# Performance work log

Hardware: AMD Instinct MI355X
Metric: run time of the kernel (lower is better)

The kernel has to match this reference:

```python
import jax, jax.numpy as jnp
import numpy as np

B, S, D = 2, 2048, 2048
H, KV, HD = 32, 8, 64          # n_heads, n_kv_heads, head_dim
NREP = H // KV                 # GQA repeat factor
ROPE_THETA = 500000.0          # llama3 base


def setup_inputs() -> dict:
    key = jax.random.key(0)
    ks = jax.random.split(key, 5)
    scale = 1.0 / np.sqrt(D)
    x = jax.random.normal(ks[0], (B, S, D), dtype=jnp.float32)
    wq = jax.random.normal(ks[1], (D, H * HD), dtype=jnp.float32) * scale
    wk = jax.random.normal(ks[2], (D, KV * HD), dtype=jnp.float32) * scale
    wv = jax.random.normal(ks[3], (D, KV * HD), dtype=jnp.float32) * scale
    wo = jax.random.normal(ks[4], (H * HD, D), dtype=jnp.float32) * scale
    # real rotary freqs, matching precompute_freqs_cis: angle[t, j] = t / theta^(2j/HD)
    inv_freq = 1.0 / (ROPE_THETA ** (np.arange(0, HD, 2, dtype=np.float32) / HD))
    t = np.arange(S, dtype=np.float32)
    ang = np.outer(t, inv_freq)  # (S, HD//2)
    freqs_cos = jnp.asarray(np.cos(ang), dtype=jnp.float32)
    freqs_sin = jnp.asarray(np.sin(ang), dtype=jnp.float32)
    return {"x": x, "wq": wq, "wk": wk, "wv": wv, "wo": wo,
            "freqs_cos": freqs_cos, "freqs_sin": freqs_sin}


def _apply_rope(t, cos, sin):
    # t: (B, S, nh, HD); pairs (even, odd) = (real, imag) of complex number
    tr = t.reshape(*t.shape[:-1], HD // 2, 2)
    re, im = tr[..., 0], tr[..., 1]
    c = cos[None, :, None, :]   # (1, S, 1, HD//2)
    s = sin[None, :, None, :]
    out_re = re * c - im * s
    out_im = re * s + im * c
    return jnp.stack([out_re, out_im], axis=-1).reshape(t.shape)


def reference(x, wq, wk, wv, wo, freqs_cos, freqs_sin):
    bsz, seq_len, _ = x.shape
    xq = (x @ wq).reshape(bsz, seq_len, H, HD)
    xk = (x @ wk).reshape(bsz, seq_len, KV, HD)
    xv = (x @ wv).reshape(bsz, seq_len, KV, HD)
    xq = _apply_rope(xq, freqs_cos, freqs_sin)
    xk = _apply_rope(xk, freqs_cos, freqs_sin)
    # GQA without materializing repeated KV: group query heads by KV head
    q = xq.transpose(0, 2, 1, 3).reshape(bsz, KV, NREP, seq_len, HD)  # bgrqh
    k = xk.transpose(0, 2, 1, 3)                                      # bgkh over seq k
    v = xv.transpose(0, 2, 1, 3)
    scores = jnp.einsum("bgrqh,bgkh->bgrqk", q, k) / jnp.sqrt(jnp.float32(HD))
    causal = jnp.tril(jnp.ones((seq_len, seq_len), dtype=bool))
    scores = jnp.where(causal[None, None, None], scores, -jnp.inf)
    probs = jax.nn.softmax(scores.astype(jnp.float32), axis=-1).astype(q.dtype)
    out = jnp.einsum("bgrqk,bgkh->bgrqh", probs, v)
    out = out.reshape(bsz, H, seq_len, HD).transpose(0, 2, 1, 3).reshape(bsz, seq_len, H * HD)
    return out @ wo
```

## Files before the change

### kernel.cpp

```cpp
#include <hip/hip_runtime.h>
#include <hip/hip_bf16.h>

typedef __attribute__((ext_vector_type(8))) short bf16x8;
typedef __attribute__((ext_vector_type(4))) float f32x4;
typedef __attribute__((ext_vector_type(16))) float f32x16;

#define S_LEN 2048
#define DMODEL 2048
#define NH 32
#define NKV 8
#define HDIM 64
#define NQKV 3072
#define BROWS 4096
#define LOG2E 1.4426950408889634f

__device__ __forceinline__ float bf2f(unsigned short u) {
    union { unsigned int i; float f; } v; v.i = ((unsigned int)u) << 16; return v.f;
}
__device__ __forceinline__ unsigned short f2bf(float f) {
    union { float f; unsigned int i; } v; v.f = f;
    unsigned int r = v.i + 0x7fffu + ((v.i >> 16) & 1u);
    return (unsigned short)(r >> 16);
}

__device__ __forceinline__ unsigned cvtpk_bf16(float lo, float hi) {
    unsigned r;
    asm("v_cvt_pk_bf16_f32 %0, %1, %2" : "=v"(r) : "v"(lo), "v"(hi));
    return r;
}
__device__ __forceinline__ void pl32swap(unsigned &a, unsigned &b) {
    asm("v_permlane32_swap_b32 %0, %1" : "+v"(a), "+v"(b));
}
__device__ __forceinline__ float exp2_fast(float x) {
    float r;
    asm("v_exp_f32 %0, %1" : "=v"(r) : "v"(x));
    return r;
}

__device__ __forceinline__ void gload_lds16(const void* g, void* l) {
    __builtin_amdgcn_global_load_lds(
        (const __attribute__((address_space(1))) unsigned int*)(unsigned long long)g,
        (__attribute__((address_space(3))) unsigned int*)(unsigned int)(unsigned long long)l,
        16, 0, 0);
}

#define VMW(n) asm volatile("s_waitcnt vmcnt(" #n ")" ::: "memory")
#define LGW()  asm volatile("s_waitcnt lgkmcnt(0)" ::: "memory")
#define CFENCE() asm volatile("" ::: "memory")

__global__ __launch_bounds__(256) void prep_kernel(
    const float* __restrict__ x,
    const float* __restrict__ wq, const float* __restrict__ wk,
    const float* __restrict__ wv, const float* __restrict__ wo,
    unsigned short* __restrict__ xb,
    unsigned short* __restrict__ wqkvT,
    unsigned short* __restrict__ woT) {
    int bid = blockIdx.x;
    if (bid < 8192) {
        int idx = bid * 256 + threadIdx.x;
        float4 v = ((const float4*)x)[idx];
        ushort4 o;
        o.x = f2bf(v.x); o.y = f2bf(v.y); o.z = f2bf(v.z); o.w = f2bf(v.w);
        ((ushort4*)xb)[idx] = o;
        return;
    }
    bid -= 8192;
    const float* src;
    unsigned short* dst;
    int N, nx;
    if (bid < 4096)      { src = wq; dst = wqkvT;                                N = 2048; nx = 64; }
    else if (bid < 5120) { bid -= 4096; src = wk; dst = wqkvT + (size_t)2048 * DMODEL; N = 512; nx = 16; }
    else if (bid < 6144) { bid -= 5120; src = wv; dst = wqkvT + (size_t)2560 * DMODEL; N = 512; nx = 16; }
    else                 { bid -= 6144; src = wo; dst = woT;                     N = 2048; nx = 64; }
    const int K = DMODEL;
    const int n0 = (bid % nx) * 32, k0 = (bid / nx) * 32;
    __shared__ float t[32][33];
    const int tx = threadIdx.x & 31, ty = threadIdx.x >> 5;
#pragma unroll
    for (int i = 0; i < 32; i += 8)
        t[ty + i][tx] = src[(size_t)(k0 + ty + i) * N + n0 + tx];
    __syncthreads();
#pragma unroll
    for (int i = 0; i < 32; i += 8)
        dst[(size_t)(n0 + ty + i) * K + k0 + tx] = f2bf(t[tx][ty + i]);
}

__global__ void vtrans_kernel(const unsigned short* __restrict__ qkv,
                              unsigned short* __restrict__ vt) {
    __shared__ unsigned short t[32][33];
    int s0 = blockIdx.x * 32;
    int hd0 = (blockIdx.y & 1) * 32;
    int bg = blockIdx.y >> 1;
    int b = bg >> 3, g = bg & 7;
    int tx = threadIdx.x & 31, ty = threadIdx.x >> 5;
#pragma unroll
    for (int i = 0; i < 32; i += 8)
        t[ty + i][tx] = qkv[(size_t)(b * S_LEN + s0 + ty + i) * NQKV + 2560 + g * 64 + hd0 + tx];
    __syncthreads();
#pragma unroll
    for (int i = 0; i < 32; i += 8)
        vt[(size_t)(bg * 64 + hd0 + ty + i) * S_LEN + s0 + tx] = t[tx][ty + i];
}

template <int NJF, int OUTF32, int ROPE>
__global__ __launch_bounds__(512, 2) void gemm_wide_kernel(
    const unsigned short* __restrict__ A,
    const unsigned short* __restrict__ BT,
    void* __restrict__ Cv,
    const float* __restrict__ fc, const float* __restrict__ fs,
    int M, int N, int K, int nbx) {
    extern __shared__ __align__(16) unsigned short lds[];
    const int ABUF = 8192;
    const int BSTRIDE = NJF * 4096;
    const int BBASE = 2 * ABUF;

    const int nwg = gridDim.x;
    const int cpx = nwg >> 3;
    const int swz = ((int)blockIdx.x & 7) * cpx + ((int)blockIdx.x >> 3);
    const int m0 = (swz / nbx) * 128, n0 = (swz % nbx) * (NJF * 64);

    const int tid = threadIdx.x;
    const int lane = tid & 63, wid = tid >> 6;
    const int wr = wid >> 2, wc = wid & 3;
    const int l16 = lane & 15, lg = lane >> 4;

    const int sr0 = tid >> 3, sk0 = tid & 7;
    const int kc = (sk0 ^ (sr0 & 7)) * 8;
    const size_t K64 = (size_t)64 * K;
    const unsigned short* gA = A + (size_t)(m0 + sr0) * K + kc;
    const unsigned short* gB = BT + (size_t)(n0 + sr0) * K + kc;
    unsigned short* ldsA = lds + tid * 8;
    unsigned short* ldsB = lds + BBASE + tid * 8;

    f32x4 acc[4][NJF];
#pragma unroll
    for (int i = 0; i < 4; ++i)
#pragma unroll
        for (int j = 0; j < NJF; ++j)
#pragma unroll
            for (int e = 0; e < 4; ++e) acc[i][j][e] = 0.f;

    const int NT = K >> 6;
    {
        gload_lds16(gA, ldsA);
        gload_lds16(gA + K64, ldsA + 4096);
#pragma unroll
        for (int j = 0; j < NJF; ++j)
            gload_lds16(gB + (size_t)j * K64, ldsB + j * 4096);
    }

    for (int t = 0; t < NT; ++t) {
        const int cur = t & 1, nxt = cur ^ 1;
        if (t + 1 < NT) {
            gload_lds16(gA + 64, ldsA + nxt * ABUF);
            gload_lds16(gA + 64 + K64, ldsA + nxt * ABUF + 4096);
#pragma unroll
            for (int j = 0; j < NJF; ++j)
                gload_lds16(gB + 64 + (size_t)j * K64, ldsB + nxt * BSTRIDE + j * 4096);
            if constexpr (NJF == 6) { VMW(8); } else { VMW(6); }
        } else {
            VMW(0);
        }
        __builtin_amdgcn_s_barrier();
        CFENCE();

#pragma unroll
        for (int ks = 0; ks < 2; ++ks) {
            bf16x8 af[4], bfv[NJF];
#pragma unroll
            for (int mi = 0; mi < 4; ++mi) {
                const int rA = wr * 64 + mi * 16 + l16;
                af[mi] = *(const bf16x8*)(lds + cur * ABUF + rA * 64 + ((ks * 4 + lg) ^ (rA & 7)) * 8);
            }
#pragma unroll
            for (int nj = 0; nj < NJF; ++nj) {
                const int rB = nj * 64 + wc * 16 + l16;
                bfv[nj] = *(const bf16x8*)(lds + BBASE + cur * BSTRIDE + rB * 64 + ((ks * 4 + lg) ^ (rB & 7)) * 8);
            }
#pragma unroll
            for (int mi = 0; mi < 4; ++mi)
#pragma unroll
                for (int nj = 0; nj < NJF; ++nj)
                    acc[mi][nj] = __builtin_amdgcn_mfma_f32_16x16x32_bf16(
                        af[mi], bfv[nj], acc[mi][nj], 0, 0, 0);
        }
        CFENCE();
        LGW();
        __builtin_amdgcn_s_barrier();
        CFENCE();
        gA += 64;
        gB += 64;
    }

    const float QS = 0.125f * LOG2E;
    const int fidx = (wc * 16 + l16) >> 1;
    const bool evenl = !(l16 & 1);
#pragma unroll
    for (int mi = 0; mi < 4; ++mi) {
        const int row = m0 + wr * 64 + mi * 16 + lg * 4;
#pragma unroll
        for (int e = 0; e < 4; ++e) {
            if (OUTF32) {
                float* Cf = (float*)Cv;
#pragma unroll
                for (int nj = 0; nj < NJF; ++nj)
                    Cf[(size_t)(row + e) * N + n0 + nj * 64 + wc * 16 + l16] = acc[mi][nj][e];
            } else if (!ROPE) {
                unsigned short* Cb = (unsigned short*)Cv;
#pragma unroll
                for (int nj = 0; nj < NJF; ++nj)
                    Cb[(size_t)(row + e) * N + n0 + nj * 64 + wc * 16 + l16] = f2bf(acc[mi][nj][e]);
            } else {
                unsigned short* Cb = (unsigned short*)Cv;
                const int seq = (row + e) & (S_LEN - 1);
                const float c = fc[seq * 32 + fidx], s = fs[seq * 32 + fidx];
#pragma unroll
                for (int nj = 0; nj < NJF; ++nj) {
                    const int cbase = n0 + nj * 64 + wc * 16;
                    float v = acc[mi][nj][e];
                    float o;
                    if (cbase >= 2560) {
                        o = v;
                    } else {
                        float p = __shfl_xor(v, 1);
                        o = fmaf(v, c, evenl ? -(p * s) : (p * s));
                        if (cbase < 2048) o *= QS;
                    }
                    Cb[(size_t)(row + e) * N + cbase + l16] = f2bf(o);
                }
            }
        }
    }
}

template <int OUTF32>
__global__ __launch_bounds__(256) void gemm_bt_kernel(
    const unsigned short* __restrict__ A,
    const unsigned short* __restrict__ BT,
    void* __restrict__ Cv,
    int M, int N, int K) {
    __shared__ __align__(16) unsigned short Als[128 * 32];
    __shared__ __align__(16) unsigned short Bls[128 * 32];

    const int tid = threadIdx.x;
    const int lane = tid & 63;
    const int wid = tid >> 6;
    const int wr = wid >> 1, wc = wid & 1;
    const int l16 = lane & 15, lg = lane >> 4;
    const int m0 = blockIdx.y * 128, n0 = blockIdx.x * 128;

    f32x4 acc[4][4];
#pragma unroll
    for (int i = 0; i < 4; ++i)
#pragma unroll
        for (int j = 0; j < 4; ++j)
#pragma unroll
            for (int e = 0; e < 4; ++e) acc[i][j][e] = 0.f;

    const int f0 = tid, f1 = 256 + tid;
    const int ar0 = f0 >> 2, ac0 = (f0 & 3) * 8;
    const int ar1 = f1 >> 2, ac1 = (f1 & 3) * 8;
    const size_t Abase = (size_t)m0 * K;
    const size_t Bbase = (size_t)n0 * K;

    for (int k0 = 0; k0 < K; k0 += 32) {
        __syncthreads();
        gload_lds16(A + Abase + (size_t)ar0 * K + k0 + ac0, Als + f0 * 8);
        gload_lds16(A + Abase + (size_t)ar1 * K + k0 + ac1, Als + f1 * 8);
        gload_lds16(BT + Bbase + (size_t)ar0 * K + k0 + ac0, Bls + f0 * 8);
        gload_lds16(BT + Bbase + (size_t)ar1 * K + k0 + ac1, Bls + f1 * 8);
        __syncthreads();
        bf16x8 af[4], bfv[4];
#pragma unroll
        for (int i = 0; i < 4; ++i)
            af[i] = *(const bf16x8*)(Als + (wr * 64 + i * 16 + l16) * 32 + lg * 8);
#pragma unroll
        for (int j = 0; j < 4; ++j)
            bfv[j] = *(const bf16x8*)(Bls + (wc * 64 + j * 16 + l16) * 32 + lg * 8);
#pragma unroll
        for (int i = 0; i < 4; ++i)
#pragma unroll
            for (int j = 0; j < 4; ++j)
                acc[i][j] = __builtin_amdgcn_mfma_f32_16x16x32_bf16(af[i], bfv[j], acc[i][j], 0, 0, 0);
    }

    const int row_base = m0 + wr * 64 + lg * 4;
    const int col_base = n0 + wc * 64 + l16;
    if (OUTF32) {
        float* Cf = (float*)Cv;
#pragma unroll
        for (int i = 0; i < 4; ++i)
#pragma unroll
            for (int r = 0; r < 4; ++r)
#pragma unroll
                for (int j = 0; j < 4; ++j)
                    Cf[(size_t)(row_base + i * 16 + r) * N + col_base + j * 16] = acc[i][j][r];
    } else {
        unsigned short* Cb = (unsigned short*)Cv;
#pragma unroll
        for (int i = 0; i < 4; ++i)
#pragma unroll
            for (int r = 0; r < 4; ++r)
#pragma unroll
                for (int j = 0; j < 4; ++j)
                    Cb[(size_t)(row_base + i * 16 + r) * N + col_base + j * 16] = f2bf(acc[i][j][r]);
    }
}

__global__ void rope_kernel(unsigned short* __restrict__ qkv,
                            const float* __restrict__ fc, const float* __restrict__ fs) {
    const int PAIRS = 1280;
    int idx = blockIdx.x * blockDim.x + threadIdx.x;
    int row = idx / PAIRS;
    int w = idx - row * PAIRS;
    int s = row & (S_LEN - 1);
    int col = (w < 1024) ? (w * 2) : (2048 + (w - 1024) * 2);
    int f = (col & 63) >> 1;
    float c = fc[s * 32 + f], sn = fs[s * 32 + f];
    unsigned int* p = (unsigned int*)(qkv + (size_t)row * NQKV + col);
    unsigned int v = *p;
    float re = bf2f((unsigned short)(v & 0xffffu));
    float im = bf2f((unsigned short)(v >> 16));
    float oro = re * c - im * sn;
    float oim = re * sn + im * c;
    if (w < 1024) { oro *= 0.125f * LOG2E; oim *= 0.125f * LOG2E; }
    *p = (unsigned int)f2bf(oro) | ((unsigned int)f2bf(oim) << 16);
}

__global__ __launch_bounds__(512) void attn_kernel(
    const unsigned short* __restrict__ qkv,
    const unsigned short* __restrict__ vt,
    unsigned short* __restrict__ aout) {
    __shared__ __align__(16) unsigned short Kls[2][64 * 64];
    __shared__ __align__(16) unsigned short Vls[2][64 * 64];
    __shared__ float Fbuf[8][32];

    const int tid = threadIdx.x, lane = tid & 63, wid = tid >> 6;
    const int l31 = lane & 31, hi = lane >> 5;
    const int g = blockIdx.x, b = blockIdx.y;
    const int h = g * 4 + (wid & 3);
    const int cw = wid >> 2;

    const int srow = tid >> 3, schk = tid & 7;
    const int sc = schk ^ (srow & 7);
    const unsigned short* kgs = qkv + (size_t)(b * S_LEN + srow) * NQKV + 2048 + g * 64 + sc * 8;
    const unsigned short* vgs = vt + (size_t)((b * 8 + g) * 64 + srow) * S_LEN + sc * 8;
    const int dd = tid * 8;

    const int xr = l31 & 7;

    const int z = 31 - (int)blockIdx.z;
    const int chunk = 2 * z + cw;
    const int q0 = chunk * 32;
    const int ntiles = z + 1;
    const int qg_row = q0 + l31;

    bf16x8 qf[4];
    {
        const unsigned short* qp =
            qkv + (size_t)(b * S_LEN + q0 + l31) * NQKV + h * HDIM + hi * 8;
#pragma unroll
        for (int s = 0; s < 4; ++s) qf[s] = *(const bf16x8*)(qp + s * 16);
    }

    float l_r = 0.f;
    f32x16 oacc0, oacc1;
#pragma unroll
    for (int r = 0; r < 16; ++r) { oacc0[r] = 0.f; oacc1[r] = 0.f; }

    gload_lds16(kgs, Kls[0] + dd);
    gload_lds16(vgs, Vls[0] + dd);
    __syncthreads();

    for (int t = 0; t < ntiles; ++t) {
        const int kv0 = t * 64;
        if (t + 1 < ntiles) {
            const int nkv = kv0 + 64;
            gload_lds16(kgs + (size_t)nkv * NQKV, Kls[(t + 1) & 1] + dd);
            gload_lds16(vgs + nkv, Vls[(t + 1) & 1] + dd);
        }
        const unsigned short* Kb = Kls[t & 1];
        const unsigned short* Vb = Vls[t & 1];

        f32x16 s0, s1;
#pragma unroll
        for (int r = 0; r < 16; ++r) { s0[r] = 0.f; s1[r] = 0.f; }
        __builtin_amdgcn_s_setprio(1);
#pragma unroll
        for (int s = 0; s < 4; ++s) {
            const int coff = ((s * 2 + hi) ^ xr) * 8;
            bf16x8 kf0 = *(const bf16x8*)(Kb + l31 * 64 + coff);
            bf16x8 kf1 = *(const bf16x8*)(Kb + (32 + l31) * 64 + coff);
            s0 = __builtin_amdgcn_mfma_f32_32x32x16_bf16(kf0, qf[s], s0, 0, 0, 0);
            s1 = __builtin_amdgcn_mfma_f32_32x32x16_bf16(kf1, qf[s], s1, 0, 0, 0);
        }
        __builtin_amdgcn_s_setprio(0);
        if (t == ntiles - 1) {
#pragma unroll
            for (int r = 0; r < 16; ++r) {
                int kvr = kv0 + (r & 3) + 8 * (r >> 2) + 4 * hi;
                if (kvr > qg_row) s0[r] = -3.0e38f;
                if (kvr + 32 > qg_row) s1[r] = -3.0e38f;
            }
        }
        float r0 = 0.f, r1 = 0.f, r2 = 0.f, r3 = 0.f;
#pragma unroll
        for (int r = 0; r < 16; r += 4) {
            s0[r + 0] = exp2_fast(s0[r + 0]); r0 += s0[r + 0];
            s0[r + 1] = exp2_fast(s0[r + 1]); r1 += s0[r + 1];
            s0[r + 2] = exp2_fast(s0[r + 2]); r2 += s0[r + 2];
            s0[r + 3] = exp2_fast(s0[r + 3]); r3 += s0[r + 3];
        }
#pragma unroll
        for (int r = 0; r < 16; r += 4) {
            s1[r + 0] = exp2_fast(s1[r + 0]); r0 += s1[r + 0];
            s1[r + 1] = exp2_fast(s1[r + 1]); r1 += s1[r + 1];
            s1[r + 2] = exp2_fast(s1[r + 2]); r2 += s1[r + 2];
            s1[r + 3] = exp2_fast(s1[r + 3]); r3 += s1[r + 3];
        }
        l_r += (r0 + r1) + (r2 + r3);

        unsigned pw[4][4];
#define BUILD_PA(c, S, base)                                    \
        {                                                       \
            unsigned x0 = cvtpk_bf16(S[base + 0], S[base + 1]); \
            unsigned y0 = cvtpk_bf16(S[base + 4], S[base + 5]); \
            pl32swap(x0, y0);                                   \
            unsigned x1 = cvtpk_bf16(S[base + 2], S[base + 3]); \
            unsigned y1 = cvtpk_bf16(S[base + 6], S[base + 7]); \
            pl32swap(x1, y1);                                   \
            pw[c][0] = x0; pw[c][1] = x1; pw[c][2] = y0; pw[c][3] = y1; \
        }
        BUILD_PA(0, s0, 0)
        BUILD_PA(1, s0, 8)
        BUILD_PA(2, s1, 0)
        BUILD_PA(3, s1, 8)
#undef BUILD_PA

        __builtin_amdgcn_s_setprio(1);
#pragma unroll
        for (int c = 0; c < 4; ++c) {
            union { unsigned u[4]; bf16x8 v; } pa;
            pa.u[0] = pw[c][0]; pa.u[1] = pw[c][1]; pa.u[2] = pw[c][2]; pa.u[3] = pw[c][3];
            const int coff = ((c * 2 + hi) ^ xr) * 8;
            bf16x8 vf0 = *(const bf16x8*)(Vb + l31 * 64 + coff);
            bf16x8 vf1 = *(const bf16x8*)(Vb + (32 + l31) * 64 + coff);
            oacc0 = __builtin_amdgcn_mfma_f32_32x32x16_bf16(pa.v, vf0, oacc0, 0, 0, 0);
            oacc1 = __builtin_amdgcn_mfma_f32_32x32x16_bf16(pa.v, vf1, oacc1, 0, 0, 0);
        }
        __builtin_amdgcn_s_setprio(0);
        __syncthreads();
    }

    l_r += __shfl_xor(l_r, 32);
    if (lane < 32) Fbuf[wid][l31] = 1.0f / l_r;
    asm volatile("s_waitcnt lgkmcnt(0)" ::: "memory");
#pragma unroll
    for (int rg = 0; rg < 4; ++rg) {
#pragma unroll
        for (int rr = 0; rr < 4; ++rr) {
            int row = 8 * rg + 4 * hi + rr;
            float inv = Fbuf[wid][row];
            int r = rg * 4 + rr;
            size_t orow = (size_t)(b * S_LEN + q0 + row) * DMODEL + h * HDIM;
            aout[orow + l31] = f2bf(oacc0[r] * inv);
            aout[orow + 32 + l31] = f2bf(oacc1[r] * inv);
        }
    }
}

extern "C" void kernel_launch(void* const* d_in, const int* in_sizes, int n_in,
                              void* d_out, int out_size, void* d_ws, size_t ws_size,
                              hipStream_t stream) {
    const float* x = (const float*)d_in[0];
    const float* wq = (const float*)d_in[1];
    const float* wk = (const float*)d_in[2];
    const float* wv = (const float*)d_in[3];
    const float* wo = (const float*)d_in[4];
    const float* fc = (const float*)d_in[5];
    const float* fs = (const float*)d_in[6];
    float* out = (float*)d_out;

    unsigned short* xb = (unsigned short*)d_ws;
    unsigned short* wqkvT = xb + (size_t)BROWS * DMODEL;
    unsigned short* woT = wqkvT + (size_t)NQKV * DMODEL;
    unsigned short* qkvb = woT + (size_t)DMODEL * DMODEL;
    unsigned short* aoutb = xb;
    unsigned short* vtb = wqkvT;

    hipError_t e1 = hipFuncSetAttribute(
        reinterpret_cast<const void*>(&gemm_wide_kernel<6, 0, 1>),
        hipFuncAttributeMaxDynamicSharedMemorySize, 131072);
    hipError_t e2 = hipFuncSetAttribute(
        reinterpret_cast<const void*>(&gemm_wide_kernel<4, 1, 0>),
        hipFuncAttributeMaxDynamicSharedMemorySize, 98304);
    const bool big = (e1 == hipSuccess && e2 == hipSuccess);

    prep_kernel<<<18432, 256, 0, stream>>>(x, wq, wk, wv, wo, xb, wqkvT, woT);
    if (big) {
        gemm_wide_kernel<6, 0, 1><<<(BROWS / 128) * (NQKV / 384), 512, 131072, stream>>>(
            xb, wqkvT, qkvb, fc, fs, BROWS, NQKV, DMODEL, NQKV / 384);
    } else {
        gemm_bt_kernel<0><<<dim3(NQKV / 128, BROWS / 128), 256, 0, stream>>>(
            xb, wqkvT, qkvb, BROWS, NQKV, DMODEL);
        rope_kernel<<<(BROWS * 1280) / 256, 256, 0, stream>>>(qkvb, fc, fs);
    }
    vtrans_kernel<<<dim3(S_LEN / 32, 32), 256, 0, stream>>>(qkvb, vtb);
    attn_kernel<<<dim3(NKV, 2, 32), 512, 0, stream>>>(qkvb, vtb, aoutb);
    if (big)
        gemm_wide_kernel<4, 1, 0><<<(BROWS / 128) * (DMODEL / 256), 512, 98304, stream>>>(
            aoutb, woT, out, nullptr, nullptr, BROWS, DMODEL, DMODEL, DMODEL / 256);
    else
        gemm_bt_kernel<1><<<dim3(DMODEL / 128, BROWS / 128), 256, 0, stream>>>(
            aoutb, woT, out, BROWS, DMODEL, DMODEL);
}
```

Before: 168.1 us.

## Halve GEMM K-tile to 32 with new LDS swizzle to cut shared memory

Reworks the wide GEMM kernel to stage K in chunks of 32 instead of 64. Each thread now loads one 16-byte chunk per 128 rows, and the LDS layout uses a swizzle adapted to 32-element rows. This halves dynamic LDS per workgroup (65536/49152 bytes), which may let more workgroups stay resident. The cost is twice as many loop iterations and barriers per K, with less MFMA work between synchronizations.

```diff
diff --git a/kernel.cpp b/kernel.cpp
--- a/kernel.cpp
+++ b/kernel.cpp
@@ -103,16 +103,17 @@
 }
 
 template <int NJF, int OUTF32, int ROPE>
-__global__ __launch_bounds__(512, 2) void gemm_wide_kernel(
+__global__ __launch_bounds__(512, 2) void gemm_w32_kernel(
     const unsigned short* __restrict__ A,
     const unsigned short* __restrict__ BT,
     void* __restrict__ Cv,
     const float* __restrict__ fc, const float* __restrict__ fs,
     int M, int N, int K, int nbx) {
     extern __shared__ __align__(16) unsigned short lds[];
-    const int ABUF = 8192;
-    const int BSTRIDE = NJF * 4096;
-    const int BBASE = 2 * ABUF;
+    constexpr int ABUF = 4096;
+    constexpr int BSTRIDE = NJF * 2048;
+    constexpr int BBASE = 2 * ABUF;
+    constexpr int NBL = NJF / 2;
 
     const int nwg = gridDim.x;
     const int cpx = nwg >> 3;
@@ -124,13 +125,18 @@
     const int wr = wid >> 2, wc = wid & 3;
     const int l16 = lane & 15, lg = lane >> 4;
 
-    const int sr0 = tid >> 3, sk0 = tid & 7;
-    const int kc = (sk0 ^ (sr0 & 7)) * 8;
-    const size_t K64 = (size_t)64 * K;
-    const unsigned short* gA = A + (size_t)(m0 + sr0) * K + kc;
-    const unsigned short* gB = BT + (size_t)(n0 + sr0) * K + kc;
-    unsigned short* ldsA = lds + tid * 8;
-    unsigned short* ldsB = lds + BBASE + tid * 8;
+    const int sr = tid >> 2, sk = tid & 3;
+    const int kc = (sk ^ ((sr >> 1) & 3)) * 8;
+    const size_t K128 = (size_t)128 * K;
+    const unsigned short* gA = A + (size_t)(m0 + sr) * K + kc;
+    const unsigned short* gB = BT + (size_t)(n0 + sr) * K + kc;
+
+#define WSTAGE(P, buf) do { \
+    gload_lds16(gA + (P), lds + (buf) * ABUF + tid * 8); \
+    _Pragma("unroll") for (int j = 0; j < NBL; ++j) \
+        gload_lds16(gB + (P) + (size_t)j * K128, \
+                    lds + BBASE + (buf) * BSTRIDE + j * 4096 + tid * 8); \
+} while (0)
 
     f32x4 acc[4][NJF];
 #pragma unroll
@@ -140,56 +146,41 @@
 #pragma unroll
             for (int e = 0; e < 4; ++e) acc[i][j][e] = 0.f;
 
-    const int NT = K >> 6;
-    {
-        gload_lds16(gA, ldsA);
-        gload_lds16(gA + K64, ldsA + 4096);
-#pragma unroll
-        for (int j = 0; j < NJF; ++j)
-            gload_lds16(gB + (size_t)j * K64, ldsB + j * 4096);
-    }
+    const int NT = K >> 5;
+    WSTAGE(0, 0);
 
     for (int t = 0; t < NT; ++t) {
         const int cur = t & 1, nxt = cur ^ 1;
         if (t + 1 < NT) {
-            gload_lds16(gA + 64, ldsA + nxt * ABUF);
-            gload_lds16(gA + 64 + K64, ldsA + nxt * ABUF + 4096);
-#pragma unroll
-            for (int j = 0; j < NJF; ++j)
-                gload_lds16(gB + 64 + (size_t)j * K64, ldsB + nxt * BSTRIDE + j * 4096);
-            if constexpr (NJF == 6) { VMW(8); } else { VMW(6); }
+            WSTAGE((size_t)(t + 1) * 32, nxt);
+            if constexpr (NJF == 6) { VMW(4); } else { VMW(3); }
         } else {
             VMW(0);
         }
         __builtin_amdgcn_s_barrier();
         CFENCE();
 
-#pragma unroll
-        for (int ks = 0; ks < 2; ++ks) {
-            bf16x8 af[4], bfv[NJF];
-#pragma unroll
-            for (int mi = 0; mi < 4; ++mi) {
-                const int rA = wr * 64 + mi * 16 + l16;
-                af[mi] = *(const bf16x8*)(lds + cur * ABUF + rA * 64 + ((ks * 4 + lg) ^ (rA & 7)) * 8);
-            }
-#pragma unroll
-            for (int nj = 0; nj < NJF; ++nj) {
-                const int rB = nj * 64 + wc * 16 + l16;
-                bfv[nj] = *(const bf16x8*)(lds + BBASE + cur * BSTRIDE + rB * 64 + ((ks * 4 + lg) ^ (rB & 7)) * 8);
-            }
-#pragma unroll
-            for (int mi = 0; mi < 4; ++mi)
-#pragma unroll
-                for (int nj = 0; nj < NJF; ++nj)
-                    acc[mi][nj] = __builtin_amdgcn_mfma_f32_16x16x32_bf16(
-                        af[mi], bfv[nj], acc[mi][nj], 0, 0, 0);
-        }
+        bf16x8 af[4], bfv[NJF];
+#pragma unroll
+        for (int mi = 0; mi < 4; ++mi) {
+            const int rA = wr * 64 + mi * 16 + l16;
+            af[mi] = *(const bf16x8*)(lds + cur * ABUF + rA * 32 + ((lg ^ ((rA >> 1) & 3)) * 8));
+        }
+#pragma unroll
+        for (int nj = 0; nj < NJF; ++nj) {
+            const int rB = nj * 64 + wc * 16 + l16;
+            bfv[nj] = *(const bf16x8*)(lds + BBASE + cur * BSTRIDE + rB * 32 + ((lg ^ ((rB >> 1) & 3)) * 8));
+        }
+#pragma unroll
+        for (int mi = 0; mi < 4; ++mi)
+#pragma unroll
+            for (int nj = 0; nj < NJF; ++nj)
+                acc[mi][nj] = __builtin_amdgcn_mfma_f32_16x16x32_bf16(
+                    af[mi], bfv[nj], acc[mi][nj], 0, 0, 0);
         CFENCE();
         LGW();
         __builtin_amdgcn_s_barrier();
         CFENCE();
-        gA += 64;
-        gB += 64;
     }
 
     const float QS = 0.125f * LOG2E;
@@ -231,6 +222,7 @@
             }
         }
     }
+#undef WSTAGE
 }
 
 template <int OUTF32>
@@ -489,16 +481,16 @@
     unsigned short* vtb = wqkvT;
 
     hipError_t e1 = hipFuncSetAttribute(
-        reinterpret_cast<const void*>(&gemm_wide_kernel<6, 0, 1>),
-        hipFuncAttributeMaxDynamicSharedMemorySize, 131072);
+        reinterpret_cast<const void*>(&gemm_w32_kernel<6, 0, 1>),
+        hipFuncAttributeMaxDynamicSharedMemorySize, 65536);
     hipError_t e2 = hipFuncSetAttribute(
-        reinterpret_cast<const void*>(&gemm_wide_kernel<4, 1, 0>),
-        hipFuncAttributeMaxDynamicSharedMemorySize, 98304);
+        reinterpret_cast<const void*>(&gemm_w32_kernel<4, 1, 0>),
+        hipFuncAttributeMaxDynamicSharedMemorySize, 49152);
     const bool big = (e1 == hipSuccess && e2 == hipSuccess);
 
     prep_kernel<<<18432, 256, 0, stream>>>(x, wq, wk, wv, wo, xb, wqkvT, woT);
     if (big) {
-        gemm_wide_kernel<6, 0, 1><<<(BROWS / 128) * (NQKV / 384), 512, 131072, stream>>>(
+        gemm_w32_kernel<6, 0, 1><<<(BROWS / 128) * (NQKV / 384), 512, 65536, stream>>>(
             xb, wqkvT, qkvb, fc, fs, BROWS, NQKV, DMODEL, NQKV / 384);
     } else {
         gemm_bt_kernel<0><<<dim3(NQKV / 128, BROWS / 128), 256, 0, stream>>>(
@@ -508,7 +500,7 @@
     vtrans_kernel<<<dim3(S_LEN / 32, 32), 256, 0, stream>>>(qkvb, vtb);
     attn_kernel<<<dim3(NKV, 2, 32), 512, 0, stream>>>(qkvb, vtb, aoutb);
     if (big)
-        gemm_wide_kernel<4, 1, 0><<<(BROWS / 128) * (DMODEL / 256), 512, 98304, stream>>>(
+        gemm_w32_kernel<4, 1, 0><<<(BROWS / 128) * (DMODEL / 256), 512, 49152, stream>>>(
             aoutb, woT, out, nullptr, nullptr, BROWS, DMODEL, DMODEL, DMODEL / 256);
     else
         gemm_bt_kernel<1><<<dim3(DMODEL / 128, BROWS / 128), 256, 0, stream>>>(
```

After: 175.3 us. 1.04x slower.
